# Kernel optimization log

Hardware: AMD Instinct MI355X
Metric: run time of the kernel (lower is better)

Reference implementation:

```python
import jax, jax.numpy as jnp
import numpy as np

WEIGHT = 0.1

SOBEL_X = jnp.array([[-1.,0.,1.],[-2.,0.,2.],[-1.,0.,1.]], jnp.float32).reshape(1,1,3,3)
SOBEL_Y = jnp.array([[-1.,-2.,-1.],[0.,0.,0.],[1.,2.,1.]], jnp.float32).reshape(1,1,3,3)
LAPLACIAN = jnp.array([[0.,1.,0.],[1.,-4.,1.],[0.,1.,0.]], jnp.float32).reshape(1,1,3,3)


def _conv3x3(x, k):
    # x: [B,1,H,W], k: [1,1,3,3], SAME padding (pad=1)
    return jax.lax.conv_general_dilated(x, k, (1, 1), ((1, 1), (1, 1)),
                                         dimension_numbers=('NCHW', 'OIHW', 'NCHW'))


def _extract_dem_features(dem):
    gx = _conv3x3(dem, SOBEL_X)
    gy = _conv3x3(dem, SOBEL_Y)
    gmag = jnp.sqrt(gx * gx + gy * gy + 1e-8)
    gmag = (gmag - gmag.min()) / (gmag.max() - gmag.min() + 1e-8)  # global min/max like torch
    hnorm = (dem - dem.min()) / (dem.max() - dem.min() + 1e-8)
    curv = jnp.tanh(_conv3x3(dem, LAPLACIAN) * 0.1)
    return jnp.concatenate([gmag, hnorm, curv], axis=1)  # [B,3,H,W]


def _connectivity_one(mask):
    # mask: [H,W] float32 in {0,1}; 4-connected component labeling via min-label propagation
    H, W = mask.shape
    sentinel = H * W
    fg = mask > 0
    init = jnp.where(fg, jnp.arange(H * W, dtype=jnp.int32).reshape(H, W), sentinel)

    def body(state):
        lbl, _ = state
        pad = jnp.pad(lbl, 1, constant_values=sentinel)
        nb = jnp.minimum(jnp.minimum(pad[:-2, 1:-1], pad[2:, 1:-1]),
                         jnp.minimum(pad[1:-1, :-2], pad[1:-1, 2:]))
        new = jnp.where(fg, jnp.minimum(lbl, nb), sentinel)
        return new, jnp.any(new != lbl)

    lbl, _ = jax.lax.while_loop(lambda s: s[1], body, (init, jnp.array(True)))
    sizes = jax.ops.segment_sum(mask.reshape(-1), lbl.reshape(-1), num_segments=sentinel + 1)[:sentinel]
    total = mask.sum()
    ratio = sizes.max() / jnp.maximum(total, 1.0)
    # matches scipy path: 0 if no components; (1 - main_region_ratio) otherwise
    # (single component gives ratio==1 -> 0, same as scipy's len(sizes)>1 branch)
    return jnp.where(total > 0, 1.0 - ratio, 0.0)


def _connectivity_loss(pred_prob):
    mask = (pred_prob[:, 0] > 0.5).astype(jnp.float32)  # [B,H,W]
    per_sample = jax.vmap(_connectivity_one)(mask)
    return per_sample.sum() / pred_prob.shape[0]


def _scale_consistency_loss(pred_prob):
    B, _, H, W = pred_prob.shape
    area = pred_prob.sum(axis=(1, 2, 3))
    total_pixels = H * W
    tmin, tmax = 0.1 * total_pixels, 0.3 * total_pixels
    loss = jnp.mean(jax.nn.relu(area - tmax) + jax.nn.relu(tmin - area))
    return loss / total_pixels


def reference(pred_prob, dem):
    dem_features = _extract_dem_features(dem)              # [B,3,H,W]
    pred_features = jnp.broadcast_to(pred_prob, dem_features.shape)
    similarity = jnp.mean((pred_features - dem_features) ** 2)
    conn = _connectivity_loss(pred_prob)
    scale = _scale_consistency_loss(pred_prob)
    total = similarity + 0.1 * conn + 0.05 * scale
    return WEIGHT * total


def setup_inputs() -> dict:
    key = jax.random.key(0)
    k1, k2 = jax.random.split(key)
    B, H, W = 16, 512, 512
    pred_prob = jax.random.uniform(k1, (B, 1, H, W), dtype=jnp.float32)  # post-sigmoid probs
    dem = jax.random.normal(k2, (B, 1, H, W), dtype=jnp.float32)
    return {"pred_prob": pred_prob, "dem": dem}
```

## Files before the change

kernel.cpp:

```cpp
#include <hip/hip_runtime.h>
#include <math.h>

#define IMG_B 16
#define IMG_H 512
#define IMG_W 512
#define IMG_HW (IMG_H * IMG_W)
#define NPART 4096

#define NMOM 9

#define TILES 256
#define NODES_PER_TILE 192
#define NODES_PER_IMG (TILES * NODES_PER_TILE)
#define PAIRS 128
#define TOUCH (1 << 30)

struct Scal {
    float gmin, gmax, dmin, dmax;
    double mom[NMOM];
    double area[IMG_B];
    int fgcnt[IMG_B];
    int maxcnt[IMG_B];
};

#define OFF_PMM   512
#define OFF_MOM   66048
#define OFF_FG    360960
#define OFF_SCR   377344

__device__ __forceinline__ int uf_findv(const int* L, int p) {
    while (true) { const int q = ((volatile const int*)L)[p]; if (q == p) return p; p = q; }
}
__device__ __forceinline__ void uf_merge(int* L, int a, int b) {
    while (true) {
        a = uf_findv(L, a);
        b = uf_findv(L, b);
        if (a == b) return;
        if (a < b) { int t = a; a = b; b = t; }
        const int old = atomicMin(&L[a], b);
        if (old == a) return;
        a = old;
    }
}

__device__ __forceinline__ int run_start(unsigned m, int b) {
    const unsigned below = ~m & ((b == 0) ? 0u : ((1u << b) - 1u));
    return below ? (int)(32u - (unsigned)__builtin_clz(below)) : 0;
}
__device__ __forceinline__ int run_len(unsigned m, int s) {
    const unsigned inv = ~(m >> s);
    return inv ? __builtin_ctz(inv) : (32 - s);
}
__device__ __forceinline__ int run_idx(unsigned sm, int c) {
    return __popc(sm & (unsigned)((2ull << c) - 1ull)) - 1;
}
__device__ __forceinline__ unsigned spread4(unsigned x) {
    x &= 0xFFu;
    x = (x | (x << 12)) & 0x000F000Fu;
    x = (x | (x << 6))  & 0x03030303u;
    x = (x | (x << 3))  & 0x11111111u;
    return x;
}

__device__ __forceinline__ void ring_decode(int i, int& x, int& y) {
    if (i < 32)      { x = i;      y = 0;      }
    else if (i < 64) { x = i - 32; y = 31;     }
    else if (i < 94) { x = 0;      y = i - 63; }
    else             { x = 31;     y = i - 93; }
}

__global__ void k_main(const float* __restrict__ dem, const float* __restrict__ pred,
                       float4* __restrict__ pmm, double* __restrict__ pblk,
                       int* __restrict__ pfg,
                       int* __restrict__ Lp, int* __restrict__ Cp,
                       int* __restrict__ nslot, int* __restrict__ pairmax,
                       int b0, int nloc, int featOn) {
    __shared__ double smem_d[2052];
    int* smem = (int*)smem_d;
    const int tid = threadIdx.x;
    const int lane = tid & 63, wid = tid >> 6;

    if (blockIdx.x >= 64) {
        if (!featOn) return;
        const int fb = blockIdx.x - 64;
        const int b = blockIdx.y;
        const size_t off = (size_t)b * IMG_HW;
        const float* d = dem + off;
        const float* p = pred + off;
        const int base = fb * 1024 + tid * 8;
        const int y = base >> 9;

        const float4 z4 = make_float4(0.f, 0.f, 0.f, 0.f);
        float4 m0 = *(const float4*)(d + base);
        float4 m1 = *(const float4*)(d + base + 4);
        float4 u0 = z4, u1 = z4, w0 = z4, w1 = z4;
        if (y > 0)   { u0 = *(const float4*)(d + base - 512); u1 = *(const float4*)(d + base - 508); }
        if (y < 511) { w0 = *(const float4*)(d + base + 512); w1 = *(const float4*)(d + base + 516); }

        float uu[10], mm[10], ww[10];
        { float t;
          t = __shfl(m1.w, lane - 1); mm[0] = (lane > 0)  ? t : 0.f;
          t = __shfl(m0.x, lane + 1); mm[9] = (lane < 63) ? t : 0.f;
          t = __shfl(u1.w, lane - 1); uu[0] = (lane > 0)  ? t : 0.f;
          t = __shfl(u0.x, lane + 1); uu[9] = (lane < 63) ? t : 0.f;
          t = __shfl(w1.w, lane - 1); ww[0] = (lane > 0)  ? t : 0.f;
          t = __shfl(w0.x, lane + 1); ww[9] = (lane < 63) ? t : 0.f; }
        uu[1]=u0.x; uu[2]=u0.y; uu[3]=u0.z; uu[4]=u0.w; uu[5]=u1.x; uu[6]=u1.y; uu[7]=u1.z; uu[8]=u1.w;
        mm[1]=m0.x; mm[2]=m0.y; mm[3]=m0.z; mm[4]=m0.w; mm[5]=m1.x; mm[6]=m1.y; mm[7]=m1.z; mm[8]=m1.w;
        ww[1]=w0.x; ww[2]=w0.y; ww[3]=w0.z; ww[4]=w0.w; ww[5]=w1.x; ww[6]=w1.y; ww[7]=w1.z; ww[8]=w1.w;

        const float4 p0 = *(const float4*)(p + base);
        const float4 p1 = *(const float4*)(p + base + 4);
        const float pv[8] = {p0.x, p0.y, p0.z, p0.w, p1.x, p1.y, p1.z, p1.w};

        float gmn = 3.4e38f, gmx = -3.4e38f, dmn = 3.4e38f, dmx = -3.4e38f;
        float mf[NMOM];
#pragma unroll
        for (int m = 0; m < NMOM; ++m) mf[m] = 0.f;
        int fg = 0;
#pragma unroll
        for (int j = 0; j < 8; ++j) {
            const float gx = (uu[j+2] - uu[j]) + 2.f * (mm[j+2] - mm[j]) + (ww[j+2] - ww[j]);
            const float gy = (ww[j] - uu[j]) + 2.f * (ww[j+1] - uu[j+1]) + (ww[j+2] - uu[j+2]);
            const float gm = sqrtf(gx * gx + gy * gy + 1e-8f);
            const float lap = uu[j+1] + mm[j] + mm[j+2] + ww[j+1] - 4.f * mm[j+1];
            const float cv = tanhf(lap * 0.1f);
            const float pj = pv[j], dj = mm[j+1];
            gmn = fminf(gmn, gm); gmx = fmaxf(gmx, gm);
            dmn = fminf(dmn, dj); dmx = fmaxf(dmx, dj);
            fg += (pj > 0.5f) ? 1 : 0;
            const float et = pj - cv;
            mf[0] += pj;  mf[1] += pj * pj;
            mf[2] += gm;  mf[3] += gm * gm;  mf[4] += pj * gm;
            mf[5] += dj;  mf[6] += dj * dj;  mf[7] += pj * dj;
            mf[8] += et * et;
        }

        for (int o = 32; o > 0; o >>= 1) {
            gmn = fminf(gmn, __shfl_down(gmn, o));
            gmx = fmaxf(gmx, __shfl_down(gmx, o));
            dmn = fminf(dmn, __shfl_down(dmn, o));
            dmx = fmaxf(dmx, __shfl_down(dmx, o));
#pragma unroll
            for (int m = 0; m < NMOM; ++m) mf[m] += __shfl_down(mf[m], o);
            fg += __shfl_down(fg, o);
        }
        double (*sa)[NMOM] = (double(*)[NMOM])smem_d;
        float* sg0 = (float*)(smem_d + 18);
        float* sg1 = sg0 + 2; float* sd0 = sg0 + 4; float* sd1 = sg0 + 6;
        int* sf = (int*)(sg0 + 8);
        if (lane == 0) {
            sg0[wid] = gmn; sg1[wid] = gmx; sd0[wid] = dmn; sd1[wid] = dmx; sf[wid] = fg;
#pragma unroll
            for (int m = 0; m < NMOM; ++m) sa[wid][m] = (double)mf[m];
        }
        __syncthreads();
        if (tid == 0) {
            double mo[NMOM];
#pragma unroll
            for (int m = 0; m < NMOM; ++m) mo[m] = sa[0][m] + sa[1][m];
            gmn = fminf(gmn, sg0[1]); gmx = fmaxf(gmx, sg1[1]);
            dmn = fminf(dmn, sd0[1]); dmx = fmaxf(dmx, sd1[1]);
            fg += sf[1];
            const int bid = b * 256 + fb;
            pmm[bid] = make_float4(gmn, gmx, dmn, dmx);
#pragma unroll
            for (int m = 0; m < NMOM; ++m) pblk[(size_t)bid * NMOM + m] = mo[m];
            pfg[bid] = fg;
        }
        return;
    }

    if (blockIdx.y >= nloc) return;
    const int slot = blockIdx.y;
    const float* p = pred + (size_t)(b0 + slot) * IMG_HW;
    int* L = Lp + (size_t)slot * NODES_PER_IMG;
    int* C = Cp + (size_t)slot * NODES_PER_IMG;
    const int pair = blockIdx.x * 2 + wid;
    const int tile0 = pair * 2;
    const int half = lane >> 5;
    const int tile = tile0 + half;
    const int tx0 = (tile0 & 15) * 32;
    const int ty  = (tile0 >> 4) * 32;
    const int r = lane & 31;

    int* lab  = smem;
    int* lcnt = smem + 2048;
    int* ns   = smem + 4096;
    int* labw = lab + wid * 1024;
    int* lcw  = lcnt + wid * 1024;
    int* nsw  = ns + wid * 2;
    if (lane < 2) nsw[lane] = 0;
    const int nbase = half * 512;

    const int myit = r >> 2;
    unsigned long long q0 = 0, q1 = 0, q2 = 0, q3 = 0;
    for (int it = 0; it < 8; ++it) {
        const int row = it * 4 + (lane >> 4);
        const float4 v = *(const float4*)(p + (ty + row) * IMG_W + tx0 + (lane & 15) * 4);
        const unsigned long long t0 = __ballot(v.x > 0.5f);
        const unsigned long long t1 = __ballot(v.y > 0.5f);
        const unsigned long long t2 = __ballot(v.z > 0.5f);
        const unsigned long long t3 = __ballot(v.w > 0.5f);
        if (it == myit) { q0 = t0; q1 = t1; q2 = t2; q3 = t3; }
    }
#pragma unroll
    for (int k = 0; k < 16; ++k) {
        const int n = k * 64 + lane;
        labw[n] = n; lcw[n] = 0;
    }
    const int sh = 16 * (r & 3) + 8 * half;
    const unsigned m = spread4((unsigned)(q0 >> sh))
                     | (spread4((unsigned)(q1 >> sh)) << 1)
                     | (spread4((unsigned)(q2 >> sh)) << 2)
                     | (spread4((unsigned)(q3 >> sh)) << 3);
    const int mpl = __shfl((int)m, lane - 1);
    const unsigned mp = (r >= 1) ? (unsigned)mpl : 0u;

    const unsigned sm  = m  & ~(m << 1);
    const unsigned smp = mp & ~(mp << 1);

    if (r >= 1) {
        unsigned ov = m & mp;
        while (ov) {
            const int bpos = __builtin_ctz(ov);
            const int sa2 = run_start(m, bpos);
            const int ea = sa2 + run_len(m, sa2) - 1;
            const int sb = run_start(mp, bpos);
            const int eb = sb + run_len(mp, sb) - 1;
            uf_merge(labw, nbase + run_idx(sm, sa2) * 32 + r,
                            nbase + run_idx(smp, sb) * 32 + (r - 1));
            const int e = (ea < eb) ? ea : eb;
            ov = (e >= 31) ? 0u : (ov & ~((1u << (e + 1)) - 1u));
        }
    }

    {
        unsigned rs = sm; int j = 0;
        while (rs) {
            const int st = __builtin_ctz(rs); rs &= rs - 1;
            const int len = run_len(m, st);
            const int e = st + len - 1;
            const int node = nbase + j * 32 + r; ++j;
            const int root = uf_findv(labw, node);
            if (root != node) labw[node] = root;
            atomicAdd(&lcw[root], len);
            if (r == 0 || r == 31 || st == 0 || e == 31)
                atomicOr(&lcw[root], TOUCH);
        }
    }

    int locmax = 0;
    {
        unsigned rs = sm; int j = 0;
        while (rs) {
            rs &= rs - 1;
            const int node = nbase + j * 32 + r; ++j;
            if (labw[node] != node) continue;
            const int c = lcw[node];
            if (c & TOUCH) {
                const int sl = atomicAdd(&nsw[half], 1);
                const int gn = tile * NODES_PER_TILE + 128 + sl;
                L[gn] = gn;
                C[gn] = c & ~TOUCH;
                lcw[node] = gn;
            } else {
                locmax = max(locmax, c);
            }
        }
    }
    for (int o = 32; o > 0; o >>= 1) locmax = max(locmax, __shfl_down(locmax, o));

#pragma unroll
    for (int t = 0; t < 4; ++t) {
        const int i = lane + t * 64;
        const int h = i >> 7, idx = i & 127;
        const int tb = (tile0 + h) * NODES_PER_TILE;
        if (idx < 124) {
            int x, yy;
            ring_decode(idx, x, yy);
            const unsigned my = (unsigned)__shfl((int)m, h * 32 + yy);
            int val = -1;
            if ((my >> x) & 1u) {
                const unsigned smy = my & ~(my << 1);
                const int node = h * 512 + run_idx(smy, x) * 32 + yy;
                const int root = uf_findv(labw, node);
                val = lcw[root];
            }
            L[tb + idx] = val;
        } else {
            L[tb + idx] = -1;
        }
    }

    if (lane == 0) pairmax[slot * PAIRS + pair] = locmax;
    if (lane < 2) nslot[slot * TILES + tile0 + lane] = nsw[lane];
}

__global__ void k_red(const float4* __restrict__ pmm, const double* __restrict__ pblk,
                      const int* __restrict__ pfg, Scal* s) {
    const int wid = threadIdx.x >> 6, lane = threadIdx.x & 63;
    if (blockIdx.x < IMG_B) {
        const int b = blockIdx.x;
        const int k = b * 256 + threadIdx.x;
        double ar = pblk[(size_t)k * NMOM + 0];
        int fg = pfg[k];
        for (int o = 32; o > 0; o >>= 1) { ar += __shfl_down(ar, o); fg += __shfl_down(fg, o); }
        __shared__ double sa[4];
        __shared__ int sf[4];
        if (lane == 0) { sa[wid] = ar; sf[wid] = fg; }
        __syncthreads();
        if (threadIdx.x == 0) {
            for (int w = 1; w < 4; ++w) { ar += sa[w]; fg += sf[w]; }
            s->area[b] = ar; s->fgcnt[b] = fg;
            s->maxcnt[b] = 0;
        }
    } else if (blockIdx.x == IMG_B) {
        float gmn = 3.4e38f, gmx = -3.4e38f, dmn = 3.4e38f, dmx = -3.4e38f;
        for (int k = threadIdx.x; k < NPART; k += 256) {
            const float4 v = pmm[k];
            gmn = fminf(gmn, v.x); gmx = fmaxf(gmx, v.y);
            dmn = fminf(dmn, v.z); dmx = fmaxf(dmx, v.w);
        }
        for (int o = 32; o > 0; o >>= 1) {
            gmn = fminf(gmn, __shfl_down(gmn, o));
            gmx = fmaxf(gmx, __shfl_down(gmx, o));
            dmn = fminf(dmn, __shfl_down(dmn, o));
            dmx = fmaxf(dmx, __shfl_down(dmx, o));
        }
        __shared__ float sg0[4], sg1[4], sd0[4], sd1[4];
        if (lane == 0) { sg0[wid] = gmn; sg1[wid] = gmx; sd0[wid] = dmn; sd1[wid] = dmx; }
        __syncthreads();
        if (threadIdx.x == 0) {
            for (int w = 1; w < 4; ++w) {
                gmn = fminf(gmn, sg0[w]); gmx = fmaxf(gmx, sg1[w]);
                dmn = fminf(dmn, sd0[w]); dmx = fmaxf(dmx, sd1[w]);
            }
            s->gmin = gmn; s->gmax = gmx; s->dmin = dmn; s->dmax = dmx;
        }
    } else {
        const int m = blockIdx.x - IMG_B - 1;
        double acc = 0.0;
        for (int k = threadIdx.x; k < NPART; k += 256) acc += pblk[(size_t)k * NMOM + m];
        for (int o = 32; o > 0; o >>= 1) acc += __shfl_down(acc, o);
        __shared__ double sa[4];
        if (lane == 0) sa[wid] = acc;
        __syncthreads();
        if (threadIdx.x == 0) {
            for (int w = 1; w < 4; ++w) acc += sa[w];
            s->mom[m] = acc;
        }
    }
}

__global__ void k_bmerge(int* __restrict__ Lp) {
    const int slot = blockIdx.y;
    int* L = Lp + (size_t)slot * NODES_PER_IMG;
    const int e = blockIdx.x * 256 + threadIdx.x;
    int a, b;
    if (e < 7680) {
        const int sc = e / 512, y = e - sc * 512;
        const int ly = y & 31;
        const int tL = (y >> 5) * 16 + sc;
        const int iL = (ly == 0) ? 31 : (ly == 31) ? 63 : (93 + ly);
        const int iR = (ly == 0) ? 0  : (ly == 31) ? 32 : (63 + ly);
        a = tL * NODES_PER_TILE + iL;
        b = (tL + 1) * NODES_PER_TILE + iR;
    } else {
        const int e2 = e - 7680;
        const int sr = e2 / 512, x = e2 - sr * 512;
        const int lx = x & 31;
        const int tT = sr * 16 + (x >> 5);
        a = tT * NODES_PER_TILE + 32 + lx;
        b = (tT + 16) * NODES_PER_TILE + lx;
    }
    if (L[a] >= 0 && L[b] >= 0) uf_merge(L, a, b);
}

__global__ void k_tail(const int* __restrict__ Lp, int* __restrict__ Cp,
                       const int* __restrict__ nslot, const int* __restrict__ pairmax,
                       Scal* s, int b0) {
    const int img = blockIdx.y;
    int m = 0;
    if (blockIdx.x < 64) {
        const int* L = Lp + (size_t)img * NODES_PER_IMG;
        int* C = Cp + (size_t)img * NODES_PER_IMG;
        const int sidx = blockIdx.x * 256 + threadIdx.x;
        const int tile = sidx >> 6, sl = sidx & 63;
        if (sl < nslot[img * TILES + tile]) {
            const int g = tile * NODES_PER_TILE + 128 + sl;
            const int sz = C[g];
            const int rt = uf_findv(L, g);
            if (rt != g) m = atomicAdd(&C[rt], sz) + sz;
            else         m = sz;
        }
    } else {
        if (threadIdx.x < PAIRS) m = pairmax[img * PAIRS + threadIdx.x];
    }
    for (int o = 32; o > 0; o >>= 1) m = max(m, __shfl_down(m, o));
    __shared__ int sm[4];
    const int wid = threadIdx.x >> 6, lane = threadIdx.x & 63;
    if (lane == 0) sm[wid] = m;
    __syncthreads();
    if (threadIdx.x == 0) {
        for (int w = 1; w < 4; ++w) m = max(m, sm[w]);
        if (m > 0) atomicMax(&s->maxcnt[b0 + img], m);
    }
}

__global__ void k_final(const Scal* __restrict__ s, float* __restrict__ out) {
    const double N = (double)IMG_B * (double)IMG_HW;
    const float gdenf = s->gmax - s->gmin + 1e-8f;
    const float ddenf = s->dmax - s->dmin + 1e-8f;
    const double a = 1.0 / (double)gdenf, bb = 1.0 / (double)ddenf;
    const double gmin = (double)s->gmin, dmin = (double)s->dmin;
    const double S_p = s->mom[0], S_pp = s->mom[1];
    const double S_g = s->mom[2], S_gg = s->mom[3], S_pg = s->mom[4];
    const double S_d = s->mom[5], S_dd = s->mom[6], S_pd = s->mom[7];
    const double S_t = s->mom[8];
    const double sum_g = S_pp - 2.0 * a * (S_pg - gmin * S_p)
                       + a * a * (S_gg - 2.0 * gmin * S_g + gmin * gmin * N);
    const double sum_d = S_pp - 2.0 * bb * (S_pd - dmin * S_p)
                       + bb * bb * (S_dd - 2.0 * dmin * S_d + dmin * dmin * N);
    const double sim = (sum_g + sum_d + S_t) / (3.0 * N);

    const double tp = (double)IMG_HW;
    const double tmin = 0.1 * tp, tmax = 0.3 * tp;
    double conn = 0.0, scale = 0.0;
    for (int b = 0; b < IMG_B; ++b) {
        const int total = s->fgcnt[b];
        if (total > 0) conn += 1.0 - (double)s->maxcnt[b] / (double)total;
        const double ar = s->area[b];
        scale += fmax(ar - tmax, 0.0) + fmax(tmin - ar, 0.0);
    }
    conn /= (double)IMG_B;
    scale = (scale / (double)IMG_B) / tp;
    const double total = sim + 0.1 * conn + 0.05 * scale;
    out[0] = (float)(0.1 * total);
}

extern "C" void kernel_launch(void* const* d_in, const int* in_sizes, int n_in,
                              void* d_out, int out_size, void* d_ws, size_t ws_size,
                              hipStream_t stream) {
    const float* pred = (const float*)d_in[0];
    const float* dem  = (const float*)d_in[1];
    float* out = (float*)d_out;

    char* ws = (char*)d_ws;
    Scal* s = (Scal*)ws;
    float4* pmm  = (float4*)(ws + OFF_PMM);
    double* pblk = (double*)(ws + OFF_MOM);
    int*    pfg  = (int*)(ws + OFF_FG);
    int* scratch = (int*)(ws + OFF_SCR);
    const size_t avail_ints = (ws_size > OFF_SCR) ? (ws_size - OFF_SCR) / 4 : 0;
    const size_t per_img = 2ull * NODES_PER_IMG + TILES + PAIRS;

    long long chunk = (long long)(avail_ints / per_img);
    if (chunk < 1) chunk = 1;
    if (chunk > IMG_B) chunk = IMG_B;

    for (int b0 = 0; b0 < IMG_B; b0 += (int)chunk) {
        const int n = (int)((b0 + chunk <= IMG_B) ? chunk : (IMG_B - b0));
        int* Lp      = scratch;
        int* Cp      = scratch + (size_t)chunk * NODES_PER_IMG;
        int* nslotp  = scratch + 2ull * chunk * NODES_PER_IMG;
        int* pairmax = nslotp + (size_t)chunk * TILES;
        const int featOn = (b0 == 0) ? 1 : 0;
        const int gx = featOn ? 320 : 64;
        const int gy = featOn ? IMG_B : n;
        hipLaunchKernelGGL(k_main, dim3(gx, gy), dim3(128), 0, stream,
                           dem, pred, pmm, pblk, pfg, Lp, Cp, nslotp, pairmax,
                           b0, n, featOn);
        if (b0 == 0)
            hipLaunchKernelGGL(k_red, dim3(IMG_B + 1 + NMOM), dim3(256), 0, stream,
                               pmm, pblk, pfg, s);
        hipLaunchKernelGGL(k_bmerge, dim3(60, n), dim3(256), 0, stream, Lp);
        hipLaunchKernelGGL(k_tail,   dim3(65, n), dim3(256), 0, stream,
                           Lp, Cp, nslotp, pairmax, s, b0);
    }

    hipLaunchKernelGGL(k_final, dim3(1), dim3(1), 0, stream, s, out);
}
```

Measured before the change: 68.12 us.

## Fuse reduction into boundary-merge kernel and widen feature blocks to 16 pixels per thread

Merges the k_red reduction kernel into the k_bmerge boundary-merge kernel as a single k_mid launch, removing one kernel launch and its dependency gap. The feature-extraction blocks now have each thread handle 16 pixels instead of 8, which halves the feature block count and the number of partial results to reduce. tanh is replaced by a fast exp-based formula. Halo shuffles now work per 32-lane half-row, and the more unrolled body uses more registers.

```diff
diff --git a/kernel.cpp b/kernel.cpp
--- a/kernel.cpp
+++ b/kernel.cpp
@@ -5,7 +5,7 @@
 #define IMG_H 512
 #define IMG_W 512
 #define IMG_HW (IMG_H * IMG_W)
-#define NPART 4096
+#define NPART 2048
 
 #define NMOM 9
 
@@ -24,9 +24,9 @@
 };
 
 #define OFF_PMM   512
-#define OFF_MOM   66048
-#define OFF_FG    360960
-#define OFF_SCR   377344
+#define OFF_MOM   33280
+#define OFF_FG    180736
+#define OFF_SCR   188928
 
 __device__ __forceinline__ int uf_findv(const int* L, int p) {
     while (true) { const int q = ((volatile const int*)L)[p]; if (q == p) return p; p = q; }
@@ -87,31 +87,34 @@
         const size_t off = (size_t)b * IMG_HW;
         const float* d = dem + off;
         const float* p = pred + off;
-        const int base = fb * 1024 + tid * 8;
+        const int base = fb * 2048 + tid * 16;
         const int y = base >> 9;
-
+        const int xl = lane & 31;
+
+        float4 M[4], U[4], W[4], P[4];
         const float4 z4 = make_float4(0.f, 0.f, 0.f, 0.f);
-        float4 m0 = *(const float4*)(d + base);
-        float4 m1 = *(const float4*)(d + base + 4);
-        float4 u0 = z4, u1 = z4, w0 = z4, w1 = z4;
-        if (y > 0)   { u0 = *(const float4*)(d + base - 512); u1 = *(const float4*)(d + base - 508); }
-        if (y < 511) { w0 = *(const float4*)(d + base + 512); w1 = *(const float4*)(d + base + 516); }
-
-        float uu[10], mm[10], ww[10];
+#pragma unroll
+        for (int k = 0; k < 4; ++k) {
+            M[k] = *(const float4*)(d + base + 4 * k);
+            U[k] = (y > 0)   ? *(const float4*)(d + base - 512 + 4 * k) : z4;
+            W[k] = (y < 511) ? *(const float4*)(d + base + 512 + 4 * k) : z4;
+            P[k] = *(const float4*)(p + base + 4 * k);
+        }
+        float uu[18], mm[18], ww[18], pv[16];
+#pragma unroll
+        for (int k = 0; k < 4; ++k) {
+            mm[1+4*k]=M[k].x; mm[2+4*k]=M[k].y; mm[3+4*k]=M[k].z; mm[4+4*k]=M[k].w;
+            uu[1+4*k]=U[k].x; uu[2+4*k]=U[k].y; uu[3+4*k]=U[k].z; uu[4+4*k]=U[k].w;
+            ww[1+4*k]=W[k].x; ww[2+4*k]=W[k].y; ww[3+4*k]=W[k].z; ww[4+4*k]=W[k].w;
+            pv[4*k]=P[k].x; pv[1+4*k]=P[k].y; pv[2+4*k]=P[k].z; pv[3+4*k]=P[k].w;
+        }
         { float t;
-          t = __shfl(m1.w, lane - 1); mm[0] = (lane > 0)  ? t : 0.f;
-          t = __shfl(m0.x, lane + 1); mm[9] = (lane < 63) ? t : 0.f;
-          t = __shfl(u1.w, lane - 1); uu[0] = (lane > 0)  ? t : 0.f;
-          t = __shfl(u0.x, lane + 1); uu[9] = (lane < 63) ? t : 0.f;
-          t = __shfl(w1.w, lane - 1); ww[0] = (lane > 0)  ? t : 0.f;
-          t = __shfl(w0.x, lane + 1); ww[9] = (lane < 63) ? t : 0.f; }
-        uu[1]=u0.x; uu[2]=u0.y; uu[3]=u0.z; uu[4]=u0.w; uu[5]=u1.x; uu[6]=u1.y; uu[7]=u1.z; uu[8]=u1.w;
-        mm[1]=m0.x; mm[2]=m0.y; mm[3]=m0.z; mm[4]=m0.w; mm[5]=m1.x; mm[6]=m1.y; mm[7]=m1.z; mm[8]=m1.w;
-        ww[1]=w0.x; ww[2]=w0.y; ww[3]=w0.z; ww[4]=w0.w; ww[5]=w1.x; ww[6]=w1.y; ww[7]=w1.z; ww[8]=w1.w;
-
-        const float4 p0 = *(const float4*)(p + base);
-        const float4 p1 = *(const float4*)(p + base + 4);
-        const float pv[8] = {p0.x, p0.y, p0.z, p0.w, p1.x, p1.y, p1.z, p1.w};
+          t = __shfl(mm[16], lane - 1); mm[0]  = (xl > 0)  ? t : 0.f;
+          t = __shfl(mm[1],  lane + 1); mm[17] = (xl < 31) ? t : 0.f;
+          t = __shfl(uu[16], lane - 1); uu[0]  = (xl > 0)  ? t : 0.f;
+          t = __shfl(uu[1],  lane + 1); uu[17] = (xl < 31) ? t : 0.f;
+          t = __shfl(ww[16], lane - 1); ww[0]  = (xl > 0)  ? t : 0.f;
+          t = __shfl(ww[1],  lane + 1); ww[17] = (xl < 31) ? t : 0.f; }
 
         float gmn = 3.4e38f, gmx = -3.4e38f, dmn = 3.4e38f, dmx = -3.4e38f;
         float mf[NMOM];
@@ -119,13 +122,14 @@
         for (int m = 0; m < NMOM; ++m) mf[m] = 0.f;
         int fg = 0;
 #pragma unroll
-        for (int j = 0; j < 8; ++j) {
-            const float gx = (uu[j+2] - uu[j]) + 2.f * (mm[j+2] - mm[j]) + (ww[j+2] - ww[j]);
-            const float gy = (ww[j] - uu[j]) + 2.f * (ww[j+1] - uu[j+1]) + (ww[j+2] - uu[j+2]);
+        for (int j = 1; j <= 16; ++j) {
+            const float gx = (uu[j+1] - uu[j-1]) + 2.f * (mm[j+1] - mm[j-1]) + (ww[j+1] - ww[j-1]);
+            const float gy = (ww[j-1] - uu[j-1]) + 2.f * (ww[j] - uu[j]) + (ww[j+1] - uu[j+1]);
             const float gm = sqrtf(gx * gx + gy * gy + 1e-8f);
-            const float lap = uu[j+1] + mm[j] + mm[j+2] + ww[j+1] - 4.f * mm[j+1];
-            const float cv = tanhf(lap * 0.1f);
-            const float pj = pv[j], dj = mm[j+1];
+            const float lap = uu[j] + mm[j-1] + mm[j+1] + ww[j] - 4.f * mm[j];
+            const float e2x = __expf(0.2f * lap);
+            const float cv = 1.f - 2.f / (e2x + 1.f);
+            const float pj = pv[j-1], dj = mm[j];
             gmn = fminf(gmn, gm); gmx = fmaxf(gmx, gm);
             dmn = fminf(dmn, dj); dmx = fmaxf(dmx, dj);
             fg += (pj > 0.5f) ? 1 : 0;
@@ -162,7 +166,7 @@
             gmn = fminf(gmn, sg0[1]); gmx = fmaxf(gmx, sg1[1]);
             dmn = fminf(dmn, sd0[1]); dmx = fmaxf(dmx, sd1[1]);
             fg += sf[1];
-            const int bid = b * 256 + fb;
+            const int bid = b * 128 + fb;
             pmm[bid] = make_float4(gmn, gmx, dmn, dmx);
 #pragma unroll
             for (int m = 0; m < NMOM; ++m) pblk[(size_t)bid * NMOM + m] = mo[m];
@@ -297,25 +301,55 @@
     if (lane < 2) nslot[slot * TILES + tile0 + lane] = nsw[lane];
 }
 
-__global__ void k_red(const float4* __restrict__ pmm, const double* __restrict__ pblk,
+__global__ void k_mid(int* __restrict__ Lp,
+                      const float4* __restrict__ pmm, const double* __restrict__ pblk,
                       const int* __restrict__ pfg, Scal* s) {
     const int wid = threadIdx.x >> 6, lane = threadIdx.x & 63;
-    if (blockIdx.x < IMG_B) {
-        const int b = blockIdx.x;
-        const int k = b * 256 + threadIdx.x;
-        double ar = pblk[(size_t)k * NMOM + 0];
-        int fg = pfg[k];
+    if (blockIdx.x < 60) {
+        const int slot = blockIdx.y;
+        int* L = Lp + (size_t)slot * NODES_PER_IMG;
+        const int e = blockIdx.x * 256 + threadIdx.x;
+        int a, b;
+        if (e < 7680) {
+            const int sc = e / 512, y = e - sc * 512;
+            const int ly = y & 31;
+            const int tL = (y >> 5) * 16 + sc;
+            const int iL = (ly == 0) ? 31 : (ly == 31) ? 63 : (93 + ly);
+            const int iR = (ly == 0) ? 0  : (ly == 31) ? 32 : (63 + ly);
+            a = tL * NODES_PER_TILE + iL;
+            b = (tL + 1) * NODES_PER_TILE + iR;
+        } else {
+            const int e2 = e - 7680;
+            const int sr = e2 / 512, x = e2 - sr * 512;
+            const int lx = x & 31;
+            const int tT = sr * 16 + (x >> 5);
+            a = tT * NODES_PER_TILE + 32 + lx;
+            b = (tT + 16) * NODES_PER_TILE + lx;
+        }
+        if (L[a] >= 0 && L[b] >= 0) uf_merge(L, a, b);
+        return;
+    }
+    if (blockIdx.y != 0) return;
+    const int rb = blockIdx.x - 60;
+    if (rb < IMG_B) {
+        const int b = rb;
+        double ar = 0.0; int fg = 0;
+        if (threadIdx.x < 128) {
+            const int k = b * 128 + threadIdx.x;
+            ar = pblk[(size_t)k * NMOM + 0];
+            fg = pfg[k];
+        }
         for (int o = 32; o > 0; o >>= 1) { ar += __shfl_down(ar, o); fg += __shfl_down(fg, o); }
         __shared__ double sa[4];
         __shared__ int sf[4];
         if (lane == 0) { sa[wid] = ar; sf[wid] = fg; }
         __syncthreads();
         if (threadIdx.x == 0) {
-            for (int w = 1; w < 4; ++w) { ar += sa[w]; fg += sf[w]; }
+            ar += sa[1]; fg += sf[1];
             s->area[b] = ar; s->fgcnt[b] = fg;
             s->maxcnt[b] = 0;
         }
-    } else if (blockIdx.x == IMG_B) {
+    } else if (rb == IMG_B) {
         float gmn = 3.4e38f, gmx = -3.4e38f, dmn = 3.4e38f, dmx = -3.4e38f;
         for (int k = threadIdx.x; k < NPART; k += 256) {
             const float4 v = pmm[k];
@@ -339,7 +373,7 @@
             s->gmin = gmn; s->gmax = gmx; s->dmin = dmn; s->dmax = dmx;
         }
     } else {
-        const int m = blockIdx.x - IMG_B - 1;
+        const int m = rb - IMG_B - 1;
         double acc = 0.0;
         for (int k = threadIdx.x; k < NPART; k += 256) acc += pblk[(size_t)k * NMOM + m];
         for (int o = 32; o > 0; o >>= 1) acc += __shfl_down(acc, o);
@@ -351,30 +385,6 @@
             s->mom[m] = acc;
         }
     }
-}
-
-__global__ void k_bmerge(int* __restrict__ Lp) {
-    const int slot = blockIdx.y;
-    int* L = Lp + (size_t)slot * NODES_PER_IMG;
-    const int e = blockIdx.x * 256 + threadIdx.x;
-    int a, b;
-    if (e < 7680) {
-        const int sc = e / 512, y = e - sc * 512;
-        const int ly = y & 31;
-        const int tL = (y >> 5) * 16 + sc;
-        const int iL = (ly == 0) ? 31 : (ly == 31) ? 63 : (93 + ly);
-        const int iR = (ly == 0) ? 0  : (ly == 31) ? 32 : (63 + ly);
-        a = tL * NODES_PER_TILE + iL;
-        b = (tL + 1) * NODES_PER_TILE + iR;
-    } else {
-        const int e2 = e - 7680;
-        const int sr = e2 / 512, x = e2 - sr * 512;
-        const int lx = x & 31;
-        const int tT = sr * 16 + (x >> 5);
-        a = tT * NODES_PER_TILE + 32 + lx;
-        b = (tT + 16) * NODES_PER_TILE + lx;
-    }
-    if (L[a] >= 0 && L[b] >= 0) uf_merge(L, a, b);
 }
 
 __global__ void k_tail(const int* __restrict__ Lp, int* __restrict__ Cp,
@@ -466,16 +476,14 @@
         int* nslotp  = scratch + 2ull * chunk * NODES_PER_IMG;
         int* pairmax = nslotp + (size_t)chunk * TILES;
         const int featOn = (b0 == 0) ? 1 : 0;
-        const int gx = featOn ? 320 : 64;
+        const int gx = featOn ? 192 : 64;
         const int gy = featOn ? IMG_B : n;
         hipLaunchKernelGGL(k_main, dim3(gx, gy), dim3(128), 0, stream,
                            dem, pred, pmm, pblk, pfg, Lp, Cp, nslotp, pairmax,
                            b0, n, featOn);
-        if (b0 == 0)
-            hipLaunchKernelGGL(k_red, dim3(IMG_B + 1 + NMOM), dim3(256), 0, stream,
-                               pmm, pblk, pfg, s);
-        hipLaunchKernelGGL(k_bmerge, dim3(60, n), dim3(256), 0, stream, Lp);
-        hipLaunchKernelGGL(k_tail,   dim3(65, n), dim3(256), 0, stream,
+        hipLaunchKernelGGL(k_mid, dim3(featOn ? 86 : 60, n), dim3(256), 0, stream,
+                           Lp, pmm, pblk, pfg, s);
+        hipLaunchKernelGGL(k_tail, dim3(65, n), dim3(256), 0, stream,
                            Lp, Cp, nslotp, pairmax, s, b0);
     }
 
```

Measured after the change: 67.42 us. About the same (-1.0%).
